# Kernel tuning notes

Hardware: AMD Instinct MI355X
Metric: run time of the kernel (lower is better)

The kernel has to match this reference:

```python
import jax, jax.numpy as jnp
import numpy as np

B, A = 8192, 16
HID, NK, NQ, NV = 256, 32, 32, 128
IN_DIM, CUR_HID, CUR_OUT, N_ACT = 512, 512, 128, 64
EXT_LAMBD, INT_LAMBD = 1.0, 0.5


def setup_inputs() -> dict:
    key = jax.random.key(0)
    ks = jax.random.split(key, 16)
    def w(k, i, o):
        return jax.random.normal(k, (i, o), jnp.float32) / np.sqrt(i)
    return {
        'x': jax.random.normal(ks[0], (B * A, IN_DIM), jnp.float32),
        'hidden': jax.random.normal(ks[1], (B, A, HID), jnp.float32),
        'Wk': w(ks[2], HID, NK), 'bk': jnp.zeros((NK,), jnp.float32),
        'Wv': w(ks[3], HID, NV), 'bv': jnp.zeros((NV,), jnp.float32),
        'Wq': w(ks[4], HID, NQ), 'bq': jnp.zeros((NQ,), jnp.float32),
        'Wa': w(ks[5], NQ + NK * A, A), 'ba': jnp.zeros((A,), jnp.float32),
        'Wt1': w(ks[6], IN_DIM, CUR_HID), 'bt1': jnp.zeros((CUR_HID,), jnp.float32),
        'Wt2': w(ks[7], CUR_HID, CUR_OUT), 'bt2': jnp.zeros((CUR_OUT,), jnp.float32),
        'Wp1': w(ks[8], IN_DIM, CUR_HID), 'bp1': jnp.zeros((CUR_HID,), jnp.float32),
        'Wp2': w(ks[9], CUR_HID, CUR_HID), 'bp2': jnp.zeros((CUR_HID,), jnp.float32),
        'Wp3': w(ks[10], CUR_HID, CUR_OUT), 'bp3': jnp.zeros((CUR_OUT,), jnp.float32),
        'Wc': w(ks[11], NV + HID, HID), 'bc': jnp.zeros((HID,), jnp.float32),
        'W2': w(ks[12], HID, N_ACT), 'b2': jnp.zeros((N_ACT,), jnp.float32),
    }


def _aggregate(x, hidden, Wk, bk, Wv, bv, Wq, bq, Wa, ba, Wt1, bt1, Wt2, bt2,
               Wp1, bp1, Wp2, bp2, Wp3, bp3, Wc, bc, W2, b2):
    # communicate(): per-agent key / value / query projections
    key_ = hidden @ Wk + bk          # [B, A, NK]
    value = hidden @ Wv + bv         # [B, A, NV]
    query = hidden @ Wq + bq         # [B, A, NQ]
    # torch.cat([key[:, i, :] for i in range(A)], -1) == reshape; repeat == broadcast
    flat_key = key_.reshape(B, A * NK)
    qk = jnp.concatenate(
        [query, jnp.broadcast_to(flat_key[:, None, :], (B, A, A * NK))], axis=-1)
    attn_weights = jax.nn.softmax(qk @ Wa + ba, axis=-1)   # [B, A, A]
    # intrinsic-motivation predictors (dropout p=0.5 in eval mode -> identity)
    tar = jax.nn.relu(x @ Wt1 + bt1) @ Wt2 + bt2           # [B*A, CUR_OUT]
    pred = jax.nn.relu(x @ Wp1 + bp1)
    pred = jax.nn.relu(pred @ Wp2 + bp2)
    pred = pred @ Wp3 + bp3
    int_imp = jnp.mean((tar - pred) ** 2, axis=-1).reshape(B, A)
    int_imp = jax.nn.softmax(int_imp, axis=-1)             # [B, A]
    # view(B,A,1).repeat(1,1,A).permute(0,2,1): out[b,i,j] = int_imp[b,j]
    int_mat = jnp.broadcast_to(int_imp[:, None, :], (B, A, A))
    attn = EXT_LAMBD * attn_weights + INT_LAMBD * jax.lax.stop_gradient(int_mat)
    applied = jnp.einsum('bij,bjv->biv', attn, value)      # [B, A, NV]
    comb = jax.nn.relu(jnp.concatenate([applied, hidden], axis=-1) @ Wc + bc)
    return comb @ W2 + b2                                  # [B, A, N_ACT]


def reference(x, hidden, Wk, bk, Wv, bv, Wq, bq, Wa, ba, Wt1, bt1, Wt2, bt2,
              Wp1, bp1, Wp2, bp2, Wp3, bp3, Wc, bc, W2, b2):
    return _aggregate(x, hidden, Wk, bk, Wv, bv, Wq, bq, Wa, ba, Wt1, bt1,
                      Wt2, bt2, Wp1, bp1, Wp2, bp2, Wp3, bp3, Wc, bc, W2, b2)
```

## Files before the change

kernel.cpp:

```cpp
#include <hip/hip_runtime.h>
#include <cstddef>
#include <cstdint>

typedef unsigned short ushort_t;
typedef __attribute__((ext_vector_type(4))) float f32x4;
typedef __attribute__((ext_vector_type(8))) short bf16x8;

#define BB   8192
#define AA   16
#define BA   131072

__device__ __forceinline__ float bf2f(ushort_t u) {
    union { float f; uint32_t i; } v; v.i = ((uint32_t)u) << 16; return v.f;
}
__device__ __forceinline__ ushort_t f2bf(float f) {
    union { float f; uint32_t i; } v; v.f = f;
    uint32_t r = v.i + 0x7fffu + ((v.i >> 16) & 1u);
    return (ushort_t)(r >> 16);
}
__device__ __forceinline__ void gload_lds16(const void* g, void* l) {
    __builtin_amdgcn_global_load_lds(
        (const __attribute__((address_space(1))) uint32_t*)g,
        (__attribute__((address_space(3))) uint32_t*)l, 16, 0, 0);
}

template<bool AF32, bool RELU>
__global__ __launch_bounds__(512)
void gemm256(const void* __restrict__ Ax, int lda,
             const ushort_t* __restrict__ A2, int lda2, int ksplit,
             const ushort_t* __restrict__ Bt,
             const float* __restrict__ bias,
             ushort_t* __restrict__ C, int ldc, int K, int lgx, int rpx)
{
    __shared__ ushort_t lds[32768];

    const int tid  = threadIdx.x;
    const int w    = tid >> 6;
    const int lane = tid & 63;
    const int wm   = w >> 2;
    const int wn   = w & 3;
    const int fr   = lane & 15;
    const int fq   = lane >> 4;

    const int bid  = blockIdx.x;
    const int xcd  = bid & 7;
    const int slot = bid >> 3;
    const int x    = slot & ((1 << lgx) - 1);
    const int y    = xcd * rpx + (slot >> lgx);
    const size_t brow = (size_t)y * 256;
    const int    bcol = x * 256;

    const int NT = K >> 5;

    f32x4 acc[8][4];
#pragma unroll
    for (int m = 0; m < 8; ++m)
#pragma unroll
        for (int n = 0; n < 4; ++n) acc[m][n] = (f32x4){0.f, 0.f, 0.f, 0.f};

    const int arow  = tid >> 1;
    const int ahalf = tid & 1;
    const int as    = (arow ^ (arow >> 2)) & 3;
    float4 areg[4];

    auto stage_load = [&](int k0) {
        const int base = ((k0 >> 5) & 1) << 14;
#pragma unroll
        for (int r = 0; r < 2; ++r) {
            const int gi  = r * 512 + tid;
            const int row = gi >> 2;
            const int g   = gi & 3;
            const int s   = (row ^ (row >> 2)) & 3;
            const int col = ((g ^ s) << 3);
            gload_lds16(Bt + (size_t)(bcol + row) * K + k0 + col,
                        &lds[base + 8192 + gi * 8]);
        }
        if (AF32) {
            const float* Af  = (const float*)Ax;
            const float* src = Af + (brow + arow) * (size_t)lda + k0 + ahalf * 16;
#pragma unroll
            for (int i = 0; i < 4; ++i)
                areg[i] = *(const float4*)(src + i * 4);
        } else {
#pragma unroll
            for (int r = 0; r < 2; ++r) {
                const int gi  = r * 512 + tid;
                const int row = gi >> 2;
                const int g   = gi & 3;
                const int s   = (row ^ (row >> 2)) & 3;
                const int col = ((g ^ s) << 3);
                const ushort_t* src;
                if (k0 >= ksplit)
                    src = A2 + (brow + row) * (size_t)lda2 + (k0 - ksplit) + col;
                else
                    src = (const ushort_t*)Ax + (brow + row) * (size_t)lda + k0 + col;
                gload_lds16(src, &lds[base + gi * 8]);
            }
        }
    };

    auto stage_write = [&](int k0) {
        if (AF32) {
            const int base = ((k0 >> 5) & 1) << 14;
#pragma unroll
            for (int j = 0; j < 2; ++j) {
                ushort_t tmp[8];
                const float* f = (const float*)&areg[j * 2];
#pragma unroll
                for (int e = 0; e < 8; ++e) tmp[e] = f2bf(f[e]);
                const int gl = ahalf * 2 + j;
                const int p  = gl ^ as;
                *(bf16x8*)&lds[base + (arow * 4 + p) * 8] = *(const bf16x8*)tmp;
            }
        }
    };

    stage_load(0);
    stage_write(0);
    __syncthreads();

    const int sa = (fr ^ (fr >> 2)) & 3;
    const int pc = ((fq ^ sa) & 3) << 3;

    for (int t = 0; t < NT; ++t) {
        if (t + 1 < NT) stage_load((t + 1) << 5);

        const int base = (t & 1) << 14;
        bf16x8 a[8], b[4];
#pragma unroll
        for (int m = 0; m < 8; ++m)
            a[m] = *(const bf16x8*)&lds[base + (wm * 128 + m * 16 + fr) * 32 + pc];
#pragma unroll
        for (int n = 0; n < 4; ++n)
            b[n] = *(const bf16x8*)&lds[base + 8192 + (wn * 64 + n * 16 + fr) * 32 + pc];

        __builtin_amdgcn_s_setprio(1);
#pragma unroll
        for (int m = 0; m < 8; ++m)
#pragma unroll
            for (int n = 0; n < 4; ++n)
                acc[m][n] = __builtin_amdgcn_mfma_f32_16x16x32_bf16(
                    a[m], b[n], acc[m][n], 0, 0, 0);
        __builtin_amdgcn_s_setprio(0);

        if (t + 1 < NT) stage_write((t + 1) << 5);
        __syncthreads();
    }

#pragma unroll
    for (int m = 0; m < 8; ++m) {
        const size_t rowb = brow + wm * 128 + m * 16 + fq * 4;
#pragma unroll
        for (int n = 0; n < 4; ++n) {
            const int col = bcol + wn * 64 + n * 16 + fr;
            const float bv = bias[col];
#pragma unroll
            for (int r = 0; r < 4; ++r) {
                float v = acc[m][n][r] + bv;
                if (RELU) v = fmaxf(v, 0.f);
                C[(rowb + r) * (size_t)ldc + col] = f2bf(v);
            }
        }
    }
}

template<bool OBF16, bool RELU>
__global__ __launch_bounds__(256)
void gemm_mfma(const ushort_t* __restrict__ A, int lda,
               const ushort_t* __restrict__ A2, int lda2, int ksplit,
               const ushort_t* __restrict__ Bt,
               const float* __restrict__ bias,
               void* __restrict__ C, int ldc, int N, int K, int lgx)
{
    __shared__ ushort_t As[2][128 * 64];
    __shared__ ushort_t Bs[2][128 * 64];

    const int tid  = threadIdx.x;
    const int w    = tid >> 6;
    const int lane = tid & 63;
    const int wm   = w >> 1;
    const int wn   = w & 1;

    const int bid  = blockIdx.x;
    const int xcd  = bid & 7;
    const int slot = bid >> 3;
    const int x    = slot & ((1 << lgx) - 1);
    const int y    = xcd * 128 + (slot >> lgx);
    const size_t brow = (size_t)y * 128;
    const int    bcol = x * 128;

    const int fr   = lane & 15;
    const int fq   = lane >> 4;
    const int srow = lane >> 3;
    const int scol = (lane & 7) << 3;

    f32x4 acc[4][4];
#pragma unroll
    for (int i = 0; i < 4; ++i)
#pragma unroll
        for (int j = 0; j < 4; ++j) acc[i][j] = (f32x4){0.f, 0.f, 0.f, 0.f};

    const int NT = K >> 6;

    auto stage = [&](int buf, int k0) {
#pragma unroll
        for (int i = 0; i < 4; ++i) {
            const int c = (w << 2) + i;
            const int r = (c << 3) + srow;
            const ushort_t* asrc;
            if (k0 >= ksplit)
                asrc = A2 + (brow + r) * (size_t)lda2 + (k0 - ksplit) + scol;
            else
                asrc = A  + (brow + r) * (size_t)lda  + k0 + scol;
            gload_lds16(asrc, &As[buf][(c << 9) + lane * 8]);
            gload_lds16(Bt + (size_t)(bcol + r) * K + k0 + scol,
                        &Bs[buf][(c << 9) + lane * 8]);
        }
    };

    stage(0, 0);
    __syncthreads();

    for (int t = 0; t < NT; ++t) {
        const int cur = t & 1;
        if (t + 1 < NT) stage(cur ^ 1, (t + 1) << 6);
#pragma unroll
        for (int kk = 0; kk < 2; ++kk) {
            bf16x8 a[4], b[4];
#pragma unroll
            for (int f = 0; f < 4; ++f) {
                a[f] = *(const bf16x8*)&As[cur][(wm * 64 + f * 16 + fr) * 64 + kk * 32 + fq * 8];
                b[f] = *(const bf16x8*)&Bs[cur][(wn * 64 + f * 16 + fr) * 64 + kk * 32 + fq * 8];
            }
#pragma unroll
            for (int fm = 0; fm < 4; ++fm)
#pragma unroll
                for (int fn = 0; fn < 4; ++fn)
                    acc[fm][fn] = __builtin_amdgcn_mfma_f32_16x16x32_bf16(
                        a[fm], b[fn], acc[fm][fn], 0, 0, 0);
        }
        __syncthreads();
    }

#pragma unroll
    for (int fm = 0; fm < 4; ++fm) {
        const size_t rowb = brow + wm * 64 + fm * 16 + fq * 4;
#pragma unroll
        for (int fn = 0; fn < 4; ++fn) {
            const int col = bcol + wn * 64 + fn * 16 + fr;
            if (col < N) {
                const float bv = bias[col];
#pragma unroll
                for (int r = 0; r < 4; ++r) {
                    float v = acc[fm][fn][r] + bv;
                    if (RELU) v = fmaxf(v, 0.f);
                    const size_t idx = (rowb + r) * (size_t)ldc + col;
                    if (OBF16) ((ushort_t*)C)[idx] = f2bf(v);
                    else       ((float*)C)[idx]    = v;
                }
            }
        }
    }
}

__global__ __launch_bounds__(256)
void transpose_w(const float* __restrict__ W, ushort_t* __restrict__ Wt,
                 int K, int N, int Npad)
{
    int idx = blockIdx.x * 256 + threadIdx.x;
    if (idx >= Npad * K) return;
    int n = idx / K, k = idx - n * K;
    float v = (n < N) ? W[(size_t)k * N + n] : 0.f;
    Wt[idx] = f2bf(v);
}

__global__ __launch_bounds__(256)
void transpose_wk(const float* __restrict__ W, ushort_t* __restrict__ Wt,
                  int Ksrc, int N, int ldk, int kOff, float sign)
{
    int idx = blockIdx.x * 256 + threadIdx.x;
    if (idx >= N * Ksrc) return;
    int n = idx / Ksrc, k = idx - n * Ksrc;
    Wt[(size_t)n * ldk + kOff + k] = f2bf(sign * W[(size_t)k * N + n]);
}

__global__ __launch_bounds__(256)
void conv_f32_bf16(const float* __restrict__ src, ushort_t* __restrict__ dst)
{
    size_t q = (size_t)blockIdx.x * 256 + threadIdx.x;
    float4 v = ((const float4*)src)[q];
    ushort_t* d = dst + q * 4;
    d[0] = f2bf(v.x); d[1] = f2bf(v.y); d[2] = f2bf(v.z); d[3] = f2bf(v.w);
}

__global__ void pack_cat2(const float* __restrict__ a, const float* __restrict__ b,
                          float* __restrict__ o)
{
    int j = blockIdx.x * 256 + threadIdx.x;
    if (j < 512) o[j] = a[j];
    else if (j < 1024) o[j] = b[j - 512];
}

__global__ void pack_bias(const float* __restrict__ bk, const float* __restrict__ bq,
                          const float* __restrict__ bv, float* __restrict__ pb)
{
    int j = threadIdx.x;
    float v = 0.f;
    if      (j < 32)  v = bk[j];
    else if (j < 64)  v = bq[j - 32];
    else if (j < 192) v = bv[j - 64];
    pb[j] = v;
}

__global__ void make_cbias(const float* __restrict__ bt2, const float* __restrict__ bp3,
                           float* __restrict__ cb)
{
    int j = threadIdx.x;
    cb[j] = bt2[j] - bp3[j];
}

__global__ __launch_bounds__(64)
void mse_softmax(const ushort_t* __restrict__ diff, float* __restrict__ int_imp)
{
    const int b = blockIdx.x, lane = threadIdx.x;
    __shared__ float m[AA];
    for (int a = 0; a < AA; ++a) {
        const uint32_t u = *(const uint32_t*)(diff + ((size_t)b * AA + a) * 128 + lane * 2);
        float d0 = bf2f((ushort_t)(u & 0xffff));
        float d1 = bf2f((ushort_t)(u >> 16));
        float s = d0 * d0 + d1 * d1;
#pragma unroll
        for (int off = 32; off > 0; off >>= 1) s += __shfl_down(s, off);
        if (lane == 0) m[a] = s * (1.f / 128.f);
    }
    __syncthreads();
    if (lane == 0) {
        float mx = -1e30f;
#pragma unroll
        for (int a = 0; a < AA; ++a) mx = fmaxf(mx, m[a]);
        float e[AA], den = 0.f;
#pragma unroll
        for (int a = 0; a < AA; ++a) { e[a] = __expf(m[a] - mx); den += e[a]; }
        float inv = 1.f / den;
#pragma unroll
        for (int a = 0; a < AA; ++a) int_imp[(size_t)b * AA + a] = e[a] * inv;
    }
}

__global__ __launch_bounds__(256)
void attn_apply(const ushort_t* __restrict__ kvq, const float* __restrict__ Wa,
                const float* __restrict__ ba, const float* __restrict__ iimp,
                ushort_t* __restrict__ applied)
{
    const int b = blockIdx.x, t = threadIdx.x;
    __shared__ float klds[512], qlds[512];
    __shared__ ushort_t vlds[2048];
    __shared__ float part[16][17];
    __shared__ float kp[16];
    __shared__ float attn[16][17];

    for (int i = t; i < 512; i += 256) {
        int a = i >> 5, c = i & 31;
        const size_t base = ((size_t)b * AA + a) * 192;
        klds[i] = bf2f(kvq[base + c]);
        qlds[i] = bf2f(kvq[base + 32 + c]);
    }
    for (int i = t; i < 2048; i += 256) {
        int j = i >> 7, v = i & 127;
        vlds[i] = kvq[((size_t)b * AA + j) * 192 + 64 + v];
    }
    __syncthreads();

    {
        int j = t & 15, seg = t >> 4;
        float s = 0.f;
        for (int c = seg * 32; c < seg * 32 + 32; ++c)
            s += klds[c] * Wa[(32 + c) * 16 + j];
        part[j][seg] = s;
    }
    __syncthreads();
    if (t < 16) {
        float s = 0.f;
#pragma unroll
        for (int seg = 0; seg < 16; ++seg) s += part[t][seg];
        kp[t] = s;
    }
    __syncthreads();

    {
        int i = t >> 4, j = t & 15;
        float s = 0.f;
#pragma unroll
        for (int q = 0; q < 32; ++q) s += qlds[i * 32 + q] * Wa[q * 16 + j];
        attn[i][j] = s + kp[j] + ba[j];
    }
    __syncthreads();
    if (t < 16) {
        float mx = -1e30f;
#pragma unroll
        for (int j = 0; j < 16; ++j) mx = fmaxf(mx, attn[t][j]);
        float e[16], den = 0.f;
#pragma unroll
        for (int j = 0; j < 16; ++j) { e[j] = __expf(attn[t][j] - mx); den += e[j]; }
        float inv = 1.f / den;
#pragma unroll
        for (int j = 0; j < 16; ++j)
            attn[t][j] = e[j] * inv + 0.5f * iimp[b * 16 + j];
    }
    __syncthreads();

    for (int o = t; o < 2048; o += 256) {
        int i = o >> 7, v = o & 127;
        float s = 0.f;
#pragma unroll
        for (int j = 0; j < 16; ++j) s += attn[i][j] * bf2f(vlds[j * 128 + v]);
        applied[((size_t)b * AA + i) * 128 + v] = f2bf(s);
    }
}

extern "C" void kernel_launch(void* const* d_in, const int* in_sizes, int n_in,
                              void* d_out, int out_size, void* d_ws, size_t ws_size,
                              hipStream_t stream)
{
    const float* x      = (const float*)d_in[0];
    const float* hidden = (const float*)d_in[1];
    const float* Wk  = (const float*)d_in[2];
    const float* bk  = (const float*)d_in[3];
    const float* Wv  = (const float*)d_in[4];
    const float* bv  = (const float*)d_in[5];
    const float* Wq  = (const float*)d_in[6];
    const float* bq  = (const float*)d_in[7];
    const float* Wa  = (const float*)d_in[8];
    const float* ba  = (const float*)d_in[9];
    const float* Wt1 = (const float*)d_in[10];
    const float* bt1 = (const float*)d_in[11];
    const float* Wt2 = (const float*)d_in[12];
    const float* bt2 = (const float*)d_in[13];
    const float* Wp1 = (const float*)d_in[14];
    const float* bp1 = (const float*)d_in[15];
    const float* Wp2 = (const float*)d_in[16];
    const float* bp2 = (const float*)d_in[17];
    const float* Wp3 = (const float*)d_in[18];
    const float* bp3 = (const float*)d_in[19];
    const float* Wc  = (const float*)d_in[20];
    const float* bc  = (const float*)d_in[21];
    const float* W2  = (const float*)d_in[22];
    const float* b2  = (const float*)d_in[23];

    float*    out = (float*)d_out;
    ushort_t* ws  = (ushort_t*)d_ws;

    ushort_t* ht2  = ws;
    ushort_t* hp2  = ht2 + (size_t)BA * 1024;
    ushort_t* diff = hp2 + (size_t)BA * 512;
    ushort_t* WT   = diff + (size_t)BA * 128;
    ushort_t* kvq     = ht2;
    ushort_t* applied = ht2 + (size_t)BA * 192;
    ushort_t* comb    = ht2 + (size_t)BA * 320;
    ushort_t* hiddenb = hp2;

    ushort_t* Bg1  = WT;
    ushort_t* Wp2t = Bg1  + 1024 * 512;
    ushort_t* Dt   = Wp2t + 512 * 512;
    ushort_t* Wkvq = Dt   + 128 * 1024;
    ushort_t* Wct  = Wkvq + 256 * 256;
    ushort_t* W2t  = Wct  + 256 * 384;
    float* g1bias = (float*)(W2t + 128 * 256);
    float* pbias  = g1bias + 1024;
    float* cbias  = pbias + 256;
    float* iimp   = cbias + 128;

    const dim3 blk(256);
    const int BIG = 1 << 30;

    transpose_w<<<1024, blk, 0, stream>>>(Wt1, Bg1,             512, 512, 512);
    transpose_w<<<1024, blk, 0, stream>>>(Wp1, Bg1 + 512 * 512, 512, 512, 512);
    transpose_w<<<1024, blk, 0, stream>>>(Wp2, Wp2t, 512, 512, 512);
    transpose_wk<<<256, blk, 0, stream>>>(Wt2, Dt, 512, 128, 1024, 0,    1.f);
    transpose_wk<<<256, blk, 0, stream>>>(Wp3, Dt, 512, 128, 1024, 512, -1.f);
    transpose_w<<<32,  blk, 0, stream>>>(Wk, Wkvq + 0 * 256,   256, 32, 32);
    transpose_w<<<32,  blk, 0, stream>>>(Wq, Wkvq + 32 * 256,  256, 32, 32);
    transpose_w<<<128, blk, 0, stream>>>(Wv, Wkvq + 64 * 256,  256, 128, 128);
    transpose_w<<<64,  blk, 0, stream>>>(Wk, Wkvq + 192 * 256, 256, 0, 64);
    transpose_w<<<384, blk, 0, stream>>>(Wc, Wct, 384, 256, 256);
    transpose_w<<<128, blk, 0, stream>>>(W2, W2t, 256, 64, 128);
    pack_cat2<<<4, 256, 0, stream>>>(bt1, bp1, g1bias);
    pack_bias<<<1, 256, 0, stream>>>(bk, bq, bv, pbias);
    make_cbias<<<1, 128, 0, stream>>>(bt2, bp3, cbias);

    gemm256<true, true><<<2048, 512, 0, stream>>>(
        x, 512, nullptr, 0, BIG, Bg1, g1bias, ht2, 1024, 512, 2, 64);
    gemm256<false, true><<<1024, 512, 0, stream>>>(
        ht2 + 512, 1024, nullptr, 0, BIG, Wp2t, bp2, hp2, 512, 512, 1, 64);
    gemm_mfma<true, false><<<1024, blk, 0, stream>>>(
        ht2, 1024, hp2, 512, 512, Dt, cbias, diff, 128, 128, 1024, 0);
    mse_softmax<<<BB, 64, 0, stream>>>(diff, iimp);

    conv_f32_bf16<<<32768, blk, 0, stream>>>(hidden, hiddenb);
    gemm_mfma<true, false><<<2048, blk, 0, stream>>>(
        hiddenb, 256, hiddenb, 256, BIG, Wkvq, pbias, kvq, 192, 192, 256, 1);
    attn_apply<<<BB, blk, 0, stream>>>(kvq, Wa, ba, iimp, applied);

    gemm256<false, true><<<512, 512, 0, stream>>>(
        applied, 128, hiddenb, 256, 128, Wct, bc, comb, 256, 384, 0, 64);
    gemm_mfma<false, false><<<1024, blk, 0, stream>>>(
        comb, 256, comb, 256, BIG, W2t, b2, out, 64, 64, 256, 0);
}
```

Baseline: 702.1 us.

## Replace GEMM kernel with deeper-pipelined 64-K tile variant and pre-convert x to bf16

Replaces the two-stage gemm256 with gemm8p, which uses 64-wide K tiles, 128KB of LDS double buffering, and chunked async global-to-LDS loads interleaved with MFMA quarters, synchronised by explicit vmcnt waits and barriers. The x input is now converted to bf16 in a separate pass instead of being converted inside the first GEMM. The diff GEMM and the kvq GEMM move onto the same 256-wide kernel by zero-padding their weights and biases to 256 columns, which computes extra output columns that are thrown away. The aim is to overlap memory traffic with MFMA work more fully, at the cost of an extra conversion pass, wasted padded compute and a 2-blocks-per-CU bound.

```diff
diff --git a/kernel.cpp b/kernel.cpp
--- a/kernel.cpp
+++ b/kernel.cpp
@@ -24,15 +24,15 @@
         (__attribute__((address_space(3))) uint32_t*)l, 16, 0, 0);
 }
 
-template<bool AF32, bool RELU>
-__global__ __launch_bounds__(512)
-void gemm256(const void* __restrict__ Ax, int lda,
-             const ushort_t* __restrict__ A2, int lda2, int ksplit,
-             const ushort_t* __restrict__ Bt,
-             const float* __restrict__ bias,
-             ushort_t* __restrict__ C, int ldc, int K, int lgx, int rpx)
-{
-    __shared__ ushort_t lds[32768];
+template<bool RELU>
+__global__ __launch_bounds__(512, 2)
+void gemm8p(const ushort_t* __restrict__ A, int lda,
+            const ushort_t* __restrict__ A2, int lda2, int ksplit,
+            const ushort_t* __restrict__ Bt,
+            const float* __restrict__ bias,
+            ushort_t* __restrict__ C, int ldc, int K, int lgx, int rpx)
+{
+    __shared__ ushort_t lds[65536];
 
     const int tid  = threadIdx.x;
     const int w    = tid >> 6;
@@ -50,7 +50,11 @@
     const size_t brow = (size_t)y * 256;
     const int    bcol = x * 256;
 
-    const int NT = K >> 5;
+    const int NT = K >> 6;
+    const int NI = NT >> 1;
+
+    const int srl = tid >> 3;
+    const int spg = tid & 7;
 
     f32x4 acc[8][4];
 #pragma unroll
@@ -58,93 +62,85 @@
 #pragma unroll
         for (int n = 0; n < 4; ++n) acc[m][n] = (f32x4){0.f, 0.f, 0.f, 0.f};
 
-    const int arow  = tid >> 1;
-    const int ahalf = tid & 1;
-    const int as    = (arow ^ (arow >> 2)) & 3;
-    float4 areg[4];
-
-    auto stage_load = [&](int k0) {
-        const int base = ((k0 >> 5) & 1) << 14;
-#pragma unroll
-        for (int r = 0; r < 2; ++r) {
-            const int gi  = r * 512 + tid;
-            const int row = gi >> 2;
-            const int g   = gi & 3;
-            const int s   = (row ^ (row >> 2)) & 3;
-            const int col = ((g ^ s) << 3);
-            gload_lds16(Bt + (size_t)(bcol + row) * K + k0 + col,
-                        &lds[base + 8192 + gi * 8]);
-        }
-        if (AF32) {
-            const float* Af  = (const float*)Ax;
-            const float* src = Af + (brow + arow) * (size_t)lda + k0 + ahalf * 16;
-#pragma unroll
-            for (int i = 0; i < 4; ++i)
-                areg[i] = *(const float4*)(src + i * 4);
-        } else {
-#pragma unroll
-            for (int r = 0; r < 2; ++r) {
-                const int gi  = r * 512 + tid;
-                const int row = gi >> 2;
-                const int g   = gi & 3;
-                const int s   = (row ^ (row >> 2)) & 3;
-                const int col = ((g ^ s) << 3);
-                const ushort_t* src;
-                if (k0 >= ksplit)
-                    src = A2 + (brow + row) * (size_t)lda2 + (k0 - ksplit) + col;
-                else
-                    src = (const ushort_t*)Ax + (brow + row) * (size_t)lda + k0 + col;
-                gload_lds16(src, &lds[base + gi * 8]);
+    auto stageA = [&](int T, int s, int bi) {
+        const int k0  = T << 6;
+        const int row = (srl < 32) ? s * 32 + srl : 128 + s * 32 + (srl - 32);
+        const int col = ((spg ^ (row & 7)) << 3);
+        const ushort_t* src;
+        if (k0 >= ksplit) src = A2 + (brow + row) * (size_t)lda2 + (k0 - ksplit) + col;
+        else              src = A  + (brow + row) * (size_t)lda  + k0 + col;
+        gload_lds16(src, &lds[(bi << 15) + row * 64 + spg * 8]);
+    };
+    auto stageB = [&](int T, int c, int bi) {
+        const int k0  = T << 6;
+        const int row = c * 64 + srl;
+        const int col = ((spg ^ (row & 7)) << 3);
+        gload_lds16(Bt + (size_t)(bcol + row) * K + k0 + col,
+                    &lds[(bi << 15) + 16384 + row * 64 + spg * 8]);
+    };
+
+    stageA(0, 0, 0); stageB(0, 0, 0);
+    stageA(0, 1, 0); stageB(0, 1, 0);
+    stageA(0, 2, 0); stageB(0, 2, 0);
+    stageA(0, 3, 0); stageB(0, 3, 0);
+    stageA(1, 0, 1); stageB(1, 0, 1);
+    stageA(1, 1, 1); stageB(1, 1, 1);
+    stageA(1, 2, 1); stageB(1, 2, 1);
+
+    bf16x8 breg[4][2];
+
+    for (int i = 0; i < NI; ++i) {
+        const bool more = (i + 1 < NI);
+#pragma unroll
+        for (int h = 0; h < 2; ++h) {
+            const int bufA = h << 15;
+            const int bufB = (h << 15) + 16384;
+#pragma unroll
+            for (int q = 0; q < 4; ++q) {
+                if (q == 0) {
+                    if (h == 0 || more) asm volatile("s_waitcnt vmcnt(6)" ::: "memory");
+                    else                asm volatile("s_waitcnt vmcnt(0)" ::: "memory");
+                    __builtin_amdgcn_sched_barrier(0);
+                    __builtin_amdgcn_s_barrier();
+#pragma unroll
+                    for (int n = 0; n < 4; ++n)
+#pragma unroll
+                        for (int kk = 0; kk < 2; ++kk) {
+                            const int row = wn * 64 + n * 16 + fr;
+                            const int gp  = ((kk * 4 + fq) ^ (row & 7)) << 3;
+                            breg[n][kk] = *(const bf16x8*)&lds[bufB + row * 64 + gp];
+                        }
+                }
+                bf16x8 areg[2][2];
+#pragma unroll
+                for (int j = 0; j < 2; ++j)
+#pragma unroll
+                    for (int kk = 0; kk < 2; ++kk) {
+                        const int row = wm * 128 + (2 * q + j) * 16 + fr;
+                        const int gp  = ((kk * 4 + fq) ^ (row & 7)) << 3;
+                        areg[j][kk] = *(const bf16x8*)&lds[bufA + row * 64 + gp];
+                    }
+                if (h == 0) {
+                    if (q == 0)      { stageA(2*i+1, 3, 1); stageB(2*i+1, 3, 1); }
+                    else if (more)   { stageA(2*i+2, q-1, 0); stageB(2*i+2, q-1, 0); }
+                } else {
+                    if (q == 0) { if (more) { stageA(2*i+2, 3, 0); stageB(2*i+2, 3, 0); } }
+                    else        { if (more) { stageA(2*i+3, q-1, 1); stageB(2*i+3, q-1, 1); } }
+                }
+                __builtin_amdgcn_s_barrier();
+                __builtin_amdgcn_s_setprio(1);
+#pragma unroll
+                for (int j = 0; j < 2; ++j)
+#pragma unroll
+                    for (int n = 0; n < 4; ++n)
+#pragma unroll
+                        for (int kk = 0; kk < 2; ++kk)
+                            acc[2*q+j][n] = __builtin_amdgcn_mfma_f32_16x16x32_bf16(
+                                areg[j][kk], breg[n][kk], acc[2*q+j][n], 0, 0, 0);
+                __builtin_amdgcn_s_setprio(0);
+                __builtin_amdgcn_s_barrier();
             }
         }
-    };
-
-    auto stage_write = [&](int k0) {
-        if (AF32) {
-            const int base = ((k0 >> 5) & 1) << 14;
-#pragma unroll
-            for (int j = 0; j < 2; ++j) {
-                ushort_t tmp[8];
-                const float* f = (const float*)&areg[j * 2];
-#pragma unroll
-                for (int e = 0; e < 8; ++e) tmp[e] = f2bf(f[e]);
-                const int gl = ahalf * 2 + j;
-                const int p  = gl ^ as;
-                *(bf16x8*)&lds[base + (arow * 4 + p) * 8] = *(const bf16x8*)tmp;
-            }
-        }
-    };
-
-    stage_load(0);
-    stage_write(0);
-    __syncthreads();
-
-    const int sa = (fr ^ (fr >> 2)) & 3;
-    const int pc = ((fq ^ sa) & 3) << 3;
-
-    for (int t = 0; t < NT; ++t) {
-        if (t + 1 < NT) stage_load((t + 1) << 5);
-
-        const int base = (t & 1) << 14;
-        bf16x8 a[8], b[4];
-#pragma unroll
-        for (int m = 0; m < 8; ++m)
-            a[m] = *(const bf16x8*)&lds[base + (wm * 128 + m * 16 + fr) * 32 + pc];
-#pragma unroll
-        for (int n = 0; n < 4; ++n)
-            b[n] = *(const bf16x8*)&lds[base + 8192 + (wn * 64 + n * 16 + fr) * 32 + pc];
-
-        __builtin_amdgcn_s_setprio(1);
-#pragma unroll
-        for (int m = 0; m < 8; ++m)
-#pragma unroll
-            for (int n = 0; n < 4; ++n)
-                acc[m][n] = __builtin_amdgcn_mfma_f32_16x16x32_bf16(
-                    a[m], b[n], acc[m][n], 0, 0, 0);
-        __builtin_amdgcn_s_setprio(0);
-
-        if (t + 1 < NT) stage_write((t + 1) << 5);
-        __syncthreads();
     }
 
 #pragma unroll
@@ -293,6 +289,13 @@
     d[0] = f2bf(v.x); d[1] = f2bf(v.y); d[2] = f2bf(v.z); d[3] = f2bf(v.w);
 }
 
+__global__ __launch_bounds__(256)
+void fill_zero(ushort_t* __restrict__ p, int n)
+{
+    int i = blockIdx.x * 256 + threadIdx.x;
+    if (i < n) p[i] = 0;
+}
+
 __global__ void pack_cat2(const float* __restrict__ a, const float* __restrict__ b,
                           float* __restrict__ o)
 {
@@ -316,7 +319,7 @@
                            float* __restrict__ cb)
 {
     int j = threadIdx.x;
-    cb[j] = bt2[j] - bp3[j];
+    cb[j] = (j < 128) ? (bt2[j] - bp3[j]) : 0.f;
 }
 
 __global__ __launch_bounds__(64)
@@ -325,7 +328,7 @@
     const int b = blockIdx.x, lane = threadIdx.x;
     __shared__ float m[AA];
     for (int a = 0; a < AA; ++a) {
-        const uint32_t u = *(const uint32_t*)(diff + ((size_t)b * AA + a) * 128 + lane * 2);
+        const uint32_t u = *(const uint32_t*)(diff + ((size_t)b * AA + a) * 256 + lane * 2);
         float d0 = bf2f((ushort_t)(u & 0xffff));
         float d1 = bf2f((ushort_t)(u >> 16));
         float s = d0 * d0 + d1 * d1;
@@ -361,13 +364,13 @@
 
     for (int i = t; i < 512; i += 256) {
         int a = i >> 5, c = i & 31;
-        const size_t base = ((size_t)b * AA + a) * 192;
+        const size_t base = ((size_t)b * AA + a) * 256;
         klds[i] = bf2f(kvq[base + c]);
         qlds[i] = bf2f(kvq[base + 32 + c]);
     }
     for (int i = t; i < 2048; i += 256) {
         int j = i >> 7, v = i & 127;
-        vlds[i] = kvq[((size_t)b * AA + j) * 192 + 64 + v];
+        vlds[i] = kvq[((size_t)b * AA + j) * 256 + 64 + v];
     }
     __syncthreads();
 
@@ -450,25 +453,26 @@
     float*    out = (float*)d_out;
     ushort_t* ws  = (ushort_t*)d_ws;
 
-    ushort_t* ht2  = ws;
-    ushort_t* hp2  = ht2 + (size_t)BA * 1024;
-    ushort_t* diff = hp2 + (size_t)BA * 512;
-    ushort_t* WT   = diff + (size_t)BA * 128;
-    ushort_t* kvq     = ht2;
-    ushort_t* applied = ht2 + (size_t)BA * 192;
-    ushort_t* comb    = ht2 + (size_t)BA * 320;
+    ushort_t* xb  = ws;
+    ushort_t* ht2 = xb + (size_t)BA * 512;
+    ushort_t* hp2 = ht2 + (size_t)BA * 1024;
+    ushort_t* WT  = hp2 + (size_t)BA * 512;
+    ushort_t* diff    = xb;
+    ushort_t* kvq     = xb + (size_t)BA * 256;
     ushort_t* hiddenb = hp2;
+    ushort_t* applied = ht2;
+    ushort_t* comb    = ht2 + (size_t)BA * 128;
 
     ushort_t* Bg1  = WT;
     ushort_t* Wp2t = Bg1  + 1024 * 512;
     ushort_t* Dt   = Wp2t + 512 * 512;
-    ushort_t* Wkvq = Dt   + 128 * 1024;
+    ushort_t* Wkvq = Dt   + 256 * 1024;
     ushort_t* Wct  = Wkvq + 256 * 256;
     ushort_t* W2t  = Wct  + 256 * 384;
     float* g1bias = (float*)(W2t + 128 * 256);
     float* pbias  = g1bias + 1024;
     float* cbias  = pbias + 256;
-    float* iimp   = cbias + 128;
+    float* iimp   = cbias + 256;
 
     const dim3 blk(256);
     const int BIG = 1 << 30;
@@ -478,6 +482,7 @@
     transpose_w<<<1024, blk, 0, stream>>>(Wp2, Wp2t, 512, 512, 512);
     transpose_wk<<<256, blk, 0, stream>>>(Wt2, Dt, 512, 128, 1024, 0,    1.f);
     transpose_wk<<<256, blk, 0, stream>>>(Wp3, Dt, 512, 128, 1024, 512, -1.f);
+    fill_zero<<<512, blk, 0, stream>>>(Dt + 128 * 1024, 128 * 1024);
     transpose_w<<<32,  blk, 0, stream>>>(Wk, Wkvq + 0 * 256,   256, 32, 32);
     transpose_w<<<32,  blk, 0, stream>>>(Wq, Wkvq + 32 * 256,  256, 32, 32);
     transpose_w<<<128, blk, 0, stream>>>(Wv, Wkvq + 64 * 256,  256, 128, 128);
@@ -486,22 +491,23 @@
     transpose_w<<<128, blk, 0, stream>>>(W2, W2t, 256, 64, 128);
     pack_cat2<<<4, 256, 0, stream>>>(bt1, bp1, g1bias);
     pack_bias<<<1, 256, 0, stream>>>(bk, bq, bv, pbias);
-    make_cbias<<<1, 128, 0, stream>>>(bt2, bp3, cbias);
-
-    gemm256<true, true><<<2048, 512, 0, stream>>>(
-        x, 512, nullptr, 0, BIG, Bg1, g1bias, ht2, 1024, 512, 2, 64);
-    gemm256<false, true><<<1024, 512, 0, stream>>>(
-        ht2 + 512, 1024, nullptr, 0, BIG, Wp2t, bp2, hp2, 512, 512, 1, 64);
-    gemm_mfma<true, false><<<1024, blk, 0, stream>>>(
-        ht2, 1024, hp2, 512, 512, Dt, cbias, diff, 128, 128, 1024, 0);
+    make_cbias<<<1, 256, 0, stream>>>(bt2, bp3, cbias);
+
+    conv_f32_bf16<<<65536, blk, 0, stream>>>(x, xb);
+    gemm8p<true><<<2048, 512, 0, stream>>>(
+        xb, 512, xb, 512, BIG, Bg1, g1bias, ht2, 1024, 512, 2, 64);
+    gemm8p<true><<<1024, 512, 0, stream>>>(
+        ht2 + 512, 1024, ht2 + 512, 1024, BIG, Wp2t, bp2, hp2, 512, 512, 1, 64);
+    gemm8p<false><<<512, 512, 0, stream>>>(
+        ht2, 1024, hp2, 512, 512, Dt, cbias, diff, 256, 1024, 0, 64);
     mse_softmax<<<BB, 64, 0, stream>>>(diff, iimp);
 
     conv_f32_bf16<<<32768, blk, 0, stream>>>(hidden, hiddenb);
-    gemm_mfma<true, false><<<2048, blk, 0, stream>>>(
-        hiddenb, 256, hiddenb, 256, BIG, Wkvq, pbias, kvq, 192, 192, 256, 1);
+    gemm8p<false><<<512, 512, 0, stream>>>(
+        hiddenb, 256, hiddenb, 256, BIG, Wkvq, pbias, kvq, 256, 256, 0, 64);
     attn_apply<<<BB, blk, 0, stream>>>(kvq, Wa, ba, iimp, applied);
 
-    gemm256<false, true><<<512, 512, 0, stream>>>(
+    gemm8p<true><<<512, 512, 0, stream>>>(
         applied, 128, hiddenb, 256, 128, Wct, bc, comb, 256, 384, 0, 64);
     gemm_mfma<false, false><<<1024, blk, 0, stream>>>(
         comb, 256, comb, 256, BIG, W2t, b2, out, 64, 64, 256, 0);
```

Result: faster. 645.5 us (-8.1%).
